# Optimization experiments

Measured on AMD Instinct MI355X. Metric: run time of the kernel, lower is better.

## Reference

```python
import jax, jax.numpy as jnp
import numpy as np

H = 2048            # hidden_size
HK, HV = 16, 32     # num_k_heads, num_v_heads
DK, DV = 128, 128   # head dims
KEY_DIM = HK * DK   # 2048
VAL_DIM = HV * DV   # 4096
CONV_DIM = 2 * KEY_DIM + VAL_DIM  # 8192
KW = 4              # conv kernel width
CS = 64             # chunk size
B, S = 2, 4096
EPS = 1e-6


def setup_inputs() -> dict:
    key = jax.random.key(0)
    ks = jax.random.split(key, 8)
    sc = lambda n: 1.0 / np.sqrt(n)
    return {
        "hidden_states": jax.random.normal(ks[0], (B, S, H), jnp.float32),
        "W_qkvz": jax.random.normal(ks[1], (H, 2 * KEY_DIM + 2 * VAL_DIM), jnp.float32) * sc(H),
        "W_ba": jax.random.normal(ks[2], (H, 2 * HV), jnp.float32) * sc(H),
        "conv_w": jax.random.normal(ks[3], (CONV_DIM, KW), jnp.float32) * sc(KW),
        "A_log": jnp.log(jax.random.uniform(ks[4], (HV,), jnp.float32, 1.0, 16.0)),
        "dt_bias": jax.random.normal(ks[5], (HV,), jnp.float32) * 0.1,
        "norm_weight": jnp.ones((DV,), jnp.float32),
        "W_out": jax.random.normal(ks[6], (VAL_DIM, H), jnp.float32) * sc(VAL_DIM),
    }


def l2norm(x, eps=1e-6):
    return x * jax.lax.rsqrt(jnp.sum(x * x, -1, keepdims=True) + eps)


def chunk_gated_delta_rule(q, k, v, g, beta):
    # q,k: (B,S,HV,DK); v: (B,S,HV,DV); g,beta: (B,S,HV). S divisible by CS.
    q = l2norm(q)
    k = l2norm(k)
    tr = lambda x: jnp.swapaxes(x, 1, 2).astype(jnp.float32)  # -> (B,H,S,...)
    q, k, v = tr(q), tr(k), tr(v)
    g = jnp.swapaxes(g, 1, 2).astype(jnp.float32)
    beta = jnp.swapaxes(beta, 1, 2).astype(jnp.float32)
    q = q * (1.0 / np.sqrt(DK))
    nc = S // CS
    rs = lambda x: x.reshape(B, HV, nc, CS, x.shape[-1])
    v_beta = v * beta[..., None]
    k_beta = k * beta[..., None]
    q, k, v, k_beta, v_beta = map(rs, (q, k, v, k_beta, v_beta))
    g = jnp.cumsum(g.reshape(B, HV, nc, CS), -1)
    tril = jnp.tril(jnp.ones((CS, CS), bool))
    diff = g[..., :, None] - g[..., None, :]
    decay = jnp.exp(jnp.where(tril, diff, 0.0)) * tril  # (B,H,nc,CS,CS)
    # strictly-lower A; the original sequential loop computes T = (I - A)^{-1}
    A = -jnp.tril(jnp.einsum('bhcid,bhcjd->bhcij', k_beta, k) * decay, -1)
    eye = jnp.eye(CS, dtype=jnp.float32)
    T = jax.scipy.linalg.solve_triangular(
        eye - A, jnp.broadcast_to(eye, A.shape), lower=True, unit_diagonal=True)
    v_t = jnp.einsum('bhcij,bhcjd->bhcid', T, v_beta)
    k_cumdecay = jnp.einsum('bhcij,bhcjd->bhcid', T, k_beta * jnp.exp(g)[..., None])
    strict_low = jnp.tril(jnp.ones((CS, CS), jnp.float32), -1)

    def step(state, xs):
        q_i, k_i, v_i, kc_i, g_i, dm_i = xs  # (B,H,CS,*)
        attn = jnp.einsum('bhid,bhjd->bhij', q_i, k_i) * dm_i * strict_low
        v_new = v_i - kc_i @ state
        out = (q_i * jnp.exp(g_i)[..., None]) @ state + attn @ v_new
        g_last = g_i[..., -1]
        state = state * jnp.exp(g_last)[..., None, None] + jnp.einsum(
            'bhcd,bhcv->bhdv', k_i * jnp.exp(g_last[..., None] - g_i)[..., None], v_new)
        return state, out

    S0 = jnp.zeros((B, HV, DK, DV), jnp.float32)
    mv = lambda x: jnp.moveaxis(x, 2, 0)  # chunk axis first for scan
    _, outs = jax.lax.scan(step, S0, (mv(q), mv(k), mv(v_t), mv(k_cumdecay), mv(g), mv(decay)))
    out = jnp.moveaxis(outs, 0, 2).reshape(B, HV, S, DV)
    return jnp.swapaxes(out, 1, 2)  # (B,S,HV,DV)


def reference(hidden_states, W_qkvz, W_ba, conv_w, A_log, dt_bias, norm_weight, W_out):
    r = HV // HK
    qkvz = hidden_states @ W_qkvz                     # (B,S,2*KEY+2*VAL)
    ba = hidden_states @ W_ba                         # (B,S,2*HV)
    qkvz = qkvz.reshape(B, S, HK, 2 * DK + 2 * r * DV)
    q, k, v, z = jnp.split(qkvz, [DK, 2 * DK, 2 * DK + r * DV], axis=-1)
    v = v.reshape(B, S, HV, DV)
    z = z.reshape(B, S, HV, DV)
    ba = ba.reshape(B, S, HK, 2 * r)
    b, a = jnp.split(ba, [r], axis=-1)
    b = b.reshape(B, S, HV)
    a = a.reshape(B, S, HV)
    # fused causal depthwise conv + silu over [q|k|v]
    mixed = jnp.concatenate([q.reshape(B, S, -1), k.reshape(B, S, -1), v.reshape(B, S, -1)], -1)
    x = jnp.swapaxes(mixed, 1, 2)                     # (B, CONV_DIM, S)
    xp = jnp.pad(x, ((0, 0), (0, 0), (KW - 1, 0)))
    conv = sum(conv_w[:, j][None, :, None] * xp[:, :, j:j + S] for j in range(KW))
    conv = jax.nn.silu(conv)
    qkv = jnp.swapaxes(conv, 1, 2)
    q, k, v = jnp.split(qkv, [KEY_DIM, 2 * KEY_DIM], axis=-1)
    q = q.reshape(B, S, HK, DK)
    k = k.reshape(B, S, HK, DK)
    v = v.reshape(B, S, HV, DV)
    beta = jax.nn.sigmoid(b)
    g = -jnp.exp(A_log) * jax.nn.softplus(a + dt_bias)
    q = jnp.repeat(q, r, axis=2)
    k = jnp.repeat(k, r, axis=2)
    core = chunk_gated_delta_rule(q, k, v, g, beta)   # (B,S,HV,DV)
    # gated RMSNorm over head_v_dim
    cf = core.astype(jnp.float32)
    var = jnp.mean(cf * cf, -1, keepdims=True)
    core = cf * jax.lax.rsqrt(var + EPS) * norm_weight
    core = core * jax.nn.silu(z.astype(jnp.float32))
    return core.reshape(B, S, VAL_DIM) @ W_out        # (B,S,H)
```

## Files before the change

### kernel.cpp

```cpp
#include <hip/hip_runtime.h>
#include <cstdint>
#include <cstddef>


typedef _Float16 half_t;
typedef _Float16 half2_t __attribute__((ext_vector_type(2)));
typedef _Float16 half4_t __attribute__((ext_vector_type(4)));
typedef _Float16 half8   __attribute__((ext_vector_type(8)));
typedef float    f32x4   __attribute__((ext_vector_type(4)));

#define MFMA16(a, b, c) __builtin_amdgcn_mfma_f32_16x16x32_f16((a), (b), (c), 0, 0, 0)

#define AS1 __attribute__((address_space(1)))
#define AS3 __attribute__((address_space(3)))

__device__ __forceinline__ void gload16(void* lds, const void* g) {
    __builtin_amdgcn_global_load_lds((AS1 void*)(g), (AS3 void*)(lds), 16, 0, 0);
}

__device__ __forceinline__ void at_wr(float* AT, int i, int j, float v) {
    *(float*)((char*)AT + i * 256 + ((j * 4) ^ ((i & 7) << 4))) = v;
}
__device__ __forceinline__ half8 frag64(const half_t* base, int row, int koff) {
    return *(const half8*)((const char*)base + row * 128 + ((koff * 2) ^ ((row & 7) << 4)));
}
__device__ __forceinline__ void w64(half_t* base, int row, int col, float v) {
    *(half_t*)((char*)base + row * 128 + ((col * 2) ^ ((row & 7) << 4))) = (half_t)v;
}
__device__ __forceinline__ half8 frag128(const half_t* base, int row, int koff) {
    return *(const half8*)((const char*)base + row * 256 + ((koff * 2) ^ ((row & 7) << 4)));
}

__global__ __launch_bounds__(256) void cast_h_k(const float* __restrict__ src,
                                                half_t* __restrict__ dst) {
    long i = (long)blockIdx.x * 256 + threadIdx.x;
    f32x4 v = *(const f32x4*)(src + i * 4);
    half4_t h;
    h[0] = (half_t)v[0]; h[1] = (half_t)v[1]; h[2] = (half_t)v[2]; h[3] = (half_t)v[3];
    *(half4_t*)(dst + i * 4) = h;
}

__global__ __launch_bounds__(256) void build_w1t_k(const float* __restrict__ Wq,
                                                   const float* __restrict__ Wba,
                                                   half_t* __restrict__ W1T) {
    __shared__ half_t tile[32][33];
    int n0 = blockIdx.x * 32, k0 = blockIdx.y * 32;
    int tx = threadIdx.x & 31, ty = threadIdx.x >> 5;
#pragma unroll
    for (int t = 0; t < 4; ++t) {
        int k = k0 + ty + t * 8, n = n0 + tx;
        float v = 0.f;
        if (n < 2048) {
            int kh = n >> 7, d = n & 127;
            v = Wq[(long)k * 12288 + kh * 768 + d];
        } else if (n < 4096) {
            int n2 = n - 2048; int kh = n2 >> 7, d = n2 & 127;
            v = Wq[(long)k * 12288 + kh * 768 + 128 + d];
        } else if (n < 8192) {
            int n3 = n - 4096; int vh = n3 >> 7, d = n3 & 127;
            int kh = vh >> 1, jj = vh & 1;
            v = Wq[(long)k * 12288 + kh * 768 + 256 + jj * 128 + d];
        } else if (n < 8256) {
            v = Wba[(long)k * 64 + (n - 8192)];
        } else if (n >= 8448) {
            int n4 = n - 8448; int vh = n4 >> 7, d = n4 & 127;
            int kh = vh >> 1, jj = vh & 1;
            v = Wq[(long)k * 12288 + kh * 768 + 512 + jj * 128 + d];
        }
        tile[ty + t * 8][tx] = (half_t)v;
    }
    __syncthreads();
#pragma unroll
    for (int t = 0; t < 4; ++t) {
        int n = n0 + ty + t * 8, k = k0 + tx;
        W1T[(long)n * 2048 + k] = tile[tx][ty + t * 8];
    }
}

__global__ __launch_bounds__(256) void build_wot_k(const float* __restrict__ Wo,
                                                   half_t* __restrict__ WoT) {
    __shared__ half_t tile[32][33];
    int n0 = blockIdx.x * 32, k0 = blockIdx.y * 32;
    int tx = threadIdx.x & 31, ty = threadIdx.x >> 5;
#pragma unroll
    for (int t = 0; t < 4; ++t) {
        int k = k0 + ty + t * 8, n = n0 + tx;
        tile[ty + t * 8][tx] = (half_t)Wo[(long)k * 2048 + n];
    }
    __syncthreads();
#pragma unroll
    for (int t = 0; t < 4; ++t) {
        int n = n0 + ty + t * 8, k = k0 + tx;
        WoT[(long)n * 4096 + k] = tile[tx][ty + t * 8];
    }
}

template <int OUT_F16>
__global__ __launch_bounds__(512, 2) void gemm256_k(const half_t* __restrict__ A,
                                                    const half_t* __restrict__ Bt,
                                                    void* __restrict__ C,
                                                    int K, int ldc,
                                                    int nwgM, int nwgN) {
    __shared__ half_t LA[2][2][8192];
    __shared__ half_t LB[2][2][8192];
    const int tid = threadIdx.x, lane = tid & 63, w = tid >> 6;
    const int lo = lane & 15, hi = lane >> 4;
    const int wm = w >> 2, wn = w & 3;
    const int nwg = gridDim.x, q = nwg >> 3, bid = blockIdx.x;
    const int swz = (bid & 7) * q + (bid >> 3);
    const int grp = 8 * nwgN;
    const int gid = swz / grp;
    const int rem = swz - gid * grp;
    const int fm = gid * 8;
    const int gsz = min(nwgM - fm, 8);
    const long tm = fm + rem % gsz;
    const long tn = rem / gsz;
    const long Kb = (long)K * 2;
    const char* Ab = (const char*)A + tm * 256 * Kb;
    const char* Bb = (const char*)Bt + tn * 256 * Kb;
    const int scol = ((lane & 7) << 4) ^ ((lane >> 3) << 4);
    const int srow = lane >> 3;
    const int s0 = w * 2, s1 = w * 2 + 1;

    auto stA = [&](int kt, int h) {
        char* hb = (char*)&LA[kt & 1][h][0];
        const char* gb = Ab + (long)(h * 128) * Kb + (long)kt * 128;
        gload16(hb + s0 * 1024, gb + (long)(s0 * 8 + srow) * Kb + scol);
        gload16(hb + s1 * 1024, gb + (long)(s1 * 8 + srow) * Kb + scol);
    };
    auto stB = [&](int kt, int h) {
        char* hb = (char*)&LB[kt & 1][h][0];
        const char* gb = Bb + (long)(h * 128) * Kb + (long)kt * 128;
        gload16(hb + s0 * 1024, gb + (long)(s0 * 8 + srow) * Kb + scol);
        gload16(hb + s1 * 1024, gb + (long)(s1 * 8 + srow) * Kb + scol);
    };
    auto rdA = [&](int p, int mt, int ks) -> half8 {
        int r = mt * 16 + lo;
        return *(const half8*)((const char*)&LA[p][wm][0] + r * 128 +
                               ((ks * 64 + hi * 16) ^ ((r & 7) << 4)));
    };
    auto rdB = [&](int p, int nt, int ks) -> half8 {
        int r = (wn & 1) * 64 + nt * 16 + lo;
        return *(const half8*)((const char*)&LB[p][wn >> 1][0] + r * 128 +
                               ((ks * 64 + hi * 16) ^ ((r & 7) << 4)));
    };

    f32x4 acc[8][4] = {};
    half8 af[4][2], bfa[2][2], bfb[2][2];

    auto ldsA4 = [&](int p, int mbase) {
#pragma unroll
        for (int mt = 0; mt < 4; ++mt) {
            af[mt][0] = rdA(p, mbase + mt, 0);
            af[mt][1] = rdA(p, mbase + mt, 1);
        }
    };
    auto ldsB2 = [&](int p, int nbase, half8 (&dst)[2][2]) {
#pragma unroll
        for (int nt = 0; nt < 2; ++nt) {
            dst[nt][0] = rdB(p, nbase + nt, 0);
            dst[nt][1] = rdB(p, nbase + nt, 1);
        }
    };
    auto quad = [&](const half8 (&bq)[2][2], int mo, int no) {
        __builtin_amdgcn_s_setprio(1);
#pragma unroll
        for (int mt = 0; mt < 4; ++mt)
#pragma unroll
            for (int nt = 0; nt < 2; ++nt) {
                acc[mo + mt][no + nt] = MFMA16(af[mt][0], bq[nt][0], acc[mo + mt][no + nt]);
                acc[mo + mt][no + nt] = MFMA16(af[mt][1], bq[nt][1], acc[mo + mt][no + nt]);
            }
        __builtin_amdgcn_s_setprio(0);
        __builtin_amdgcn_s_barrier();
    };

    const int nkt = K >> 6, niter = nkt >> 1;
    stA(0, 0); stA(0, 1); stB(0, 0); stB(0, 1);
    stA(1, 0); stB(1, 0); stB(1, 1);
    asm volatile("s_waitcnt vmcnt(6)" ::: "memory");
    __builtin_amdgcn_s_barrier();

    for (int i = 0; i < niter; ++i) {
        const int k0 = 2 * i, k1 = 2 * i + 1;
        const bool sa = (k0 + 2 < nkt), sb = (k1 + 2 < nkt);
        ldsA4(0, 0); ldsB2(0, 0, bfa);
        stA(k1, 1);
        __builtin_amdgcn_s_barrier();
        quad(bfa, 0, 0);
        ldsB2(0, 2, bfb);
        __builtin_amdgcn_s_barrier();
        quad(bfb, 0, 2);
        ldsA4(0, 4);
        if (sa) stB(k0 + 2, 0);
        __builtin_amdgcn_s_barrier();
        quad(bfa, 4, 0);
        if (sa) {
            stA(k0 + 2, 0); stB(k0 + 2, 1);
            asm volatile("s_waitcnt vmcnt(6)" ::: "memory");
        } else {
            asm volatile("s_waitcnt vmcnt(0)" ::: "memory");
        }
        __builtin_amdgcn_s_barrier();
        quad(bfb, 4, 2);
        ldsA4(1, 0); ldsB2(1, 0, bfa);
        if (sa) stA(k0 + 2, 1);
        __builtin_amdgcn_s_barrier();
        quad(bfa, 0, 0);
        ldsB2(1, 2, bfb);
        __builtin_amdgcn_s_barrier();
        quad(bfb, 0, 2);
        ldsA4(1, 4);
        if (sb) stB(k1 + 2, 0);
        __builtin_amdgcn_s_barrier();
        quad(bfa, 4, 0);
        if (sb) {
            stA(k1 + 2, 0); stB(k1 + 2, 1);
            asm volatile("s_waitcnt vmcnt(6)" ::: "memory");
        }
        __builtin_amdgcn_s_barrier();
        quad(bfb, 4, 2);
    }

    const long crow0 = tm * 256 + wm * 128 + hi * 4;
    const long ccol0 = tn * 256 + wn * 64 + lo;
#pragma unroll
    for (int mt = 0; mt < 8; ++mt)
#pragma unroll
        for (int nt = 0; nt < 4; ++nt)
#pragma unroll
            for (int e = 0; e < 4; ++e) {
                long row = crow0 + mt * 16 + e;
                long col = ccol0 + nt * 16;
                if (OUT_F16)
                    ((half_t*)C)[row * (long)ldc + col] = (half_t)acc[mt][nt][e];
                else
                    ((float*)C)[row * (long)ldc + col] = acc[mt][nt][e];
            }
}

__global__ __launch_bounds__(256) void conv_silu_k(const half_t* __restrict__ mixedH,
                                                   const float* __restrict__ conv_w,
                                                   half_t* __restrict__ qb,
                                                   half_t* __restrict__ kb,
                                                   half_t* __restrict__ vb) {
    int ch = blockIdx.x * 256 + threadIdx.x;
    int b = blockIdx.y >> 5, sc = blockIdx.y & 31;
    int s0 = sc * 128;
    half_t* dptr;
    long dstr;
    if (ch < 2048)      { dptr = qb + ch;          dstr = 2048; }
    else if (ch < 4096) { dptr = kb + (ch - 2048); dstr = 2048; }
    else                { dptr = vb + (ch - 4096); dstr = 4096; }
    float w0 = conv_w[ch * 4 + 0], w1 = conv_w[ch * 4 + 1];
    float w2 = conv_w[ch * 4 + 2], w3 = conv_w[ch * 4 + 3];
    const half_t* src = mixedH + (long)b * 4096 * 8448 + ch;
    float x0 = (s0 >= 3) ? (float)src[(long)(s0 - 3) * 8448] : 0.f;
    float x1 = (s0 >= 2) ? (float)src[(long)(s0 - 2) * 8448] : 0.f;
    float x2 = (s0 >= 1) ? (float)src[(long)(s0 - 1) * 8448] : 0.f;
    for (int s = s0; s < s0 + 128; ++s) {
        float x3 = (float)src[(long)s * 8448];
        float y = w0 * x0 + w1 * x1 + w2 * x2 + w3 * x3;
        y = y / (1.f + expf(-y));
        dptr[((long)b * 4096 + s) * dstr] = (half_t)y;
        x0 = x1; x1 = x2; x2 = x3;
    }
}

__global__ __launch_bounds__(256) void gate_beta_k(const half_t* __restrict__ mixedH,
                                                   const float* __restrict__ A_log,
                                                   const float* __restrict__ dt_bias,
                                                   float* __restrict__ beta,
                                                   float* __restrict__ gcum) {
    __shared__ float gs[32][64];
    int b = blockIdx.x >> 6, c = blockIdx.x & 63;
    for (int idx = threadIdx.x; idx < 2048; idx += 256) {
        int vh = idx & 31, i = idx >> 5;
        int kh = vh >> 1, j = vh & 1;
        long row = ((long)b * 4096 + c * 64 + i) * 8448 + 8192 + kh * 4;
        float bb = (float)mixedH[row + j];
        float aa = (float)mixedH[row + 2 + j];
        beta[((long)b * 4096 + c * 64 + i) * 32 + vh] = 1.f / (1.f + expf(-bb));
        float x = aa + dt_bias[vh];
        float sp = (x > 15.f) ? x : log1pf(expf(x));
        gs[vh][i] = -expf(A_log[vh]) * sp;
    }
    __syncthreads();
    if (threadIdx.x < 32) {
        int vh = threadIdx.x;
        float cum = 0.f;
        float* gout = gcum + ((long)(b * 32 + vh)) * 4096 + c * 64;
        for (int i = 0; i < 64; ++i) { cum += gs[vh][i]; gout[i] = cum; }
    }
}

__global__ __launch_bounds__(256) void l2norm_k(half_t* __restrict__ qb,
                                                half_t* __restrict__ kb) {
    int w = threadIdx.x >> 6, lane = threadIdx.x & 63;
    long rid = (long)blockIdx.x * 4 + w;
    half_t* base;
    float sc;
    if (rid < 131072) { base = qb + rid * 128; sc = 0.08838834764831845f; }
    else              { base = kb + (rid - 131072) * 128; sc = 1.f; }
    half2_t hv = *(half2_t*)(base + lane * 2);
    float f0 = (float)hv[0], f1 = (float)hv[1];
    float ss = f0 * f0 + f1 * f1;
#pragma unroll
    for (int off = 32; off; off >>= 1) ss += __shfl_xor(ss, off);
    float r = rsqrtf(ss + 1e-6f) * sc;
    half2_t o; o[0] = (half_t)(f0 * r); o[1] = (half_t)(f1 * r);
    *(half2_t*)(base + lane * 2) = o;
}

__global__ __launch_bounds__(256) void phase1_k(const half_t* __restrict__ qb,
                                                const half_t* __restrict__ kb,
                                                const half_t* __restrict__ vb,
                                                const float* __restrict__ beta,
                                                const float* __restrict__ gcum,
                                                half_t* __restrict__ attnW,
                                                half_t* __restrict__ vtW,
                                                half_t* __restrict__ kcW) {
    __shared__ float AT[64 * 64];
    __shared__ half_t XT[256 * 64];
    __shared__ float gcS[64], betaS[64], egS[64];
    int blk = blockIdx.x;
    int c = blk & 63, vh = (blk >> 6) & 31, b = blk >> 11;
    int kh = vh >> 1;
    int tid = threadIdx.x, lane = tid & 63, w = tid >> 6, lo = lane & 15, hi = lane >> 4;
    long rowbase = (long)b * 4096 + c * 64;
    if (tid < 64) {
        float g = gcum[((long)(b * 32 + vh)) * 4096 + c * 64 + tid];
        gcS[tid] = g; egS[tid] = expf(g);
        betaS[tid] = beta[(rowbase + tid) * 32 + vh];
    }
    const half_t* kR = kb + rowbase * 2048 + kh * 128;
    const half_t* qR = qb + rowbase * 2048 + kh * 128;
    f32x4 accG[4] = {}, accA[4] = {};
#pragma unroll
    for (int kt = 0; kt < 4; ++kt) {
        half8 ak = *(const half8*)(kR + (long)(w * 16 + lo) * 2048 + kt * 32 + hi * 8);
        half8 aq = *(const half8*)(qR + (long)(w * 16 + lo) * 2048 + kt * 32 + hi * 8);
#pragma unroll
        for (int n = 0; n < 4; ++n) {
            half8 bk = *(const half8*)(kR + (long)(n * 16 + lo) * 2048 + kt * 32 + hi * 8);
            accG[n] = MFMA16(ak, bk, accG[n]);
            accA[n] = MFMA16(aq, bk, accA[n]);
        }
    }
    __syncthreads();
    half_t* attnB = attnW + (long)blk * 4096;
#pragma unroll
    for (int n = 0; n < 4; ++n)
#pragma unroll
        for (int e = 0; e < 4; ++e) {
            int i = w * 16 + hi * 4 + e;
            int j = n * 16 + lo;
            float dec = (j < i) ? expf(gcS[i] - gcS[j]) : 0.f;
            float av = (j < i) ? (-betaS[i] * accG[n][e] * dec) : (j == i ? 1.f : 0.f);
            at_wr(AT, i, j, av);
            attnB[(long)i * 64 + j] = (half_t)((j < i) ? accA[n][e] * dec : 0.f);
        }
    __syncthreads();
    if (w == 0) {
        float t[64];
#pragma unroll
        for (int i = 0; i < 64; ++i) t[i] = (lane == i) ? 1.f : 0.f;
#pragma unroll
        for (int i = 1; i < 64; ++i) {
            float a0 = 0.f, a1 = 0.f, a2 = 0.f, a3 = 0.f;
#pragma unroll
            for (int p0 = 0; p0 < i; p0 += 4) {
                f32x4 a4 = *(const f32x4*)((const char*)AT + i * 256 +
                                           ((p0 * 4) ^ ((i & 7) << 4)));
                if (p0 + 0 < i) a0 += a4[0] * t[p0 + 0];
                if (p0 + 1 < i) a1 += a4[1] * t[p0 + 1];
                if (p0 + 2 < i) a2 += a4[2] * t[p0 + 2];
                if (p0 + 3 < i) a3 += a4[3] * t[p0 + 3];
            }
            t[i] += (a0 + a1) + (a2 + a3);
        }
        half_t* TS = (half_t*)AT;
#pragma unroll
        for (int i = 0; i < 64; ++i)
            *(half_t*)((char*)TS + i * 128 + ((lane * 2) ^ ((i & 7) << 4))) = (half_t)t[i];
    } else {
        for (int idx = tid - 64; idx < 4096; idx += 192) {
            int p = idx >> 6, dp = idx & 63;
            float bb = betaS[p], be = betaS[p] * egS[p];
            half2_t vv = *(const half2_t*)(vb + (rowbase + p) * 4096 + vh * 128 + dp * 2);
            half2_t kk = *(const half2_t*)(kb + (rowbase + p) * 2048 + kh * 128 + dp * 2);
            w64(XT, dp * 2,       p, (float)vv[0] * bb);
            w64(XT, dp * 2 + 1,   p, (float)vv[1] * bb);
            w64(XT, 128 + dp * 2,     p, (float)kk[0] * be);
            w64(XT, 128 + dp * 2 + 1, p, (float)kk[1] * be);
        }
    }
    __syncthreads();
    const half_t* TS = (const half_t*)AT;
    f32x4 accO[4][4] = {};
#pragma unroll
    for (int kt = 0; kt < 2; ++kt) {
        half8 tf[4];
#pragma unroll
        for (int m = 0; m < 4; ++m) tf[m] = frag64(TS, m * 16 + lo, kt * 32 + hi * 8);
#pragma unroll
        for (int n = 0; n < 4; ++n) {
            half8 bx = frag64(XT, w * 64 + n * 16 + lo, kt * 32 + hi * 8);
#pragma unroll
            for (int m = 0; m < 4; ++m) accO[m][n] = MFMA16(tf[m], bx, accO[m][n]);
        }
    }
    long ob = (long)blk * 8192;
#pragma unroll
    for (int m = 0; m < 4; ++m)
#pragma unroll
        for (int n = 0; n < 4; ++n)
#pragma unroll
            for (int e = 0; e < 4; ++e) {
                int i = m * 16 + hi * 4 + e;
                int dc = w * 64 + n * 16 + lo;
                float v = accO[m][n][e];
                if (dc < 128) vtW[ob + (long)i * 128 + dc] = (half_t)v;
                else          kcW[ob + (long)i * 128 + dc - 128] = (half_t)(-v);
            }
}

struct P2Ops {
    half8 kcf[4], qf[4], k8[4];
    half8 atf[2];
    half_t vtv[8];
    float gm, gi, g63;
};

__global__ __launch_bounds__(256, 1) void phase2_k(const half_t* __restrict__ qb,
                                                   const half_t* __restrict__ kb,
                                                   const float* __restrict__ gcum,
                                                   const half_t* __restrict__ attnW,
                                                   const half_t* __restrict__ vtW,
                                                   const half_t* __restrict__ kcW,
                                                   half_t* __restrict__ coreH) {
    __shared__ half_t SHs[32 * 128];
    __shared__ half_t vnT[32 * 64];
    __shared__ half_t kdT[128 * 64];
    int blk = blockIdx.x;
    int bvh = blk & 63, js = blk >> 6;
    int vh = bvh & 31, b = bvh >> 5, kh = vh >> 1;
    int j0 = js * 32;
    int tid = threadIdx.x, lane = tid & 63, w = tid >> 6, lo = lane & 15, hi = lane >> 4;
    int ii = tid >> 2, dseg = tid & 3;
    int jm = w >> 1, dql = (w & 1) * 4;
    for (int idx = tid; idx < 32 * 128; idx += 256) SHs[idx] = (half_t)0.f;
    __syncthreads();
    const float* gbase = gcum + (long)bvh * 4096;

    auto loadops = [&](int c, P2Ops& o) {
        long pb = (long)bvh * 64 + c;
        const half_t* kcG = kcW + pb * 8192;
        const half_t* vtG = vtW + pb * 8192;
        const half_t* atG = attnW + pb * 4096;
        long rowbase = (long)b * 4096 + c * 64;
        const float* gp = gbase + c * 64;
#pragma unroll
        for (int kt = 0; kt < 4; ++kt) {
            o.kcf[kt] = *(const half8*)(kcG + (long)(w * 16 + lo) * 128 + kt * 32 + hi * 8);
            o.qf[kt] = *(const half8*)(qb + (rowbase + w * 16 + lo) * 2048 + kh * 128 +
                                       kt * 32 + hi * 8);
        }
#pragma unroll
        for (int kt2 = 0; kt2 < 2; ++kt2)
            o.atf[kt2] = *(const half8*)(atG + (long)(w * 16 + lo) * 64 + kt2 * 32 + hi * 8);
#pragma unroll
        for (int s = 0; s < 4; ++s)
            o.k8[s] = *(const half8*)(kb + (rowbase + ii) * 2048 + kh * 128 + dseg * 32 + s * 8);
#pragma unroll
        for (int n = 0; n < 2; ++n)
#pragma unroll
            for (int e = 0; e < 4; ++e)
                o.vtv[n * 4 + e] = vtG[(long)(w * 16 + hi * 4 + e) * 128 + j0 + n * 16 + lo];
        o.gm = gp[w * 16 + lo];
        o.gi = gp[ii];
        o.g63 = gp[63];
    };

    auto step = [&](int c, P2Ops& o, P2Ops& nx) {
        long rowbase = (long)b * 4096 + c * 64;
        loadops(c + 1 < 64 ? c + 1 : 63, nx);
        half8 bS[4][2];
#pragma unroll
        for (int kt = 0; kt < 4; ++kt) {
            bS[kt][0] = frag128(SHs, lo, kt * 32 + hi * 8);
            bS[kt][1] = frag128(SHs, 16 + lo, kt * 32 + hi * 8);
        }
        f32x4 accV[2];
#pragma unroll
        for (int n = 0; n < 2; ++n)
#pragma unroll
            for (int e = 0; e < 4; ++e) accV[n][e] = (float)o.vtv[n * 4 + e];
#pragma unroll
        for (int kt = 0; kt < 4; ++kt) {
            accV[0] = MFMA16(o.kcf[kt], bS[kt][0], accV[0]);
            accV[1] = MFMA16(o.kcf[kt], bS[kt][1], accV[1]);
        }
#pragma unroll
        for (int n = 0; n < 2; ++n) {
            int j = n * 16 + lo, i0 = w * 16 + hi * 4;
            half4_t h4;
            h4[0] = (half_t)accV[n][0]; h4[1] = (half_t)accV[n][1];
            h4[2] = (half_t)accV[n][2]; h4[3] = (half_t)accV[n][3];
            *(half4_t*)((char*)vnT + j * 128 + ((i0 * 2) ^ ((j & 7) << 4))) = h4;
        }
        {
            float ek = expf(o.g63 - o.gi);
#pragma unroll
            for (int s = 0; s < 4; ++s)
#pragma unroll
                for (int e2 = 0; e2 < 8; ++e2)
                    w64(kdT, dseg * 32 + s * 8 + e2, ii, (float)o.k8[s][e2] * ek);
        }
        __syncthreads();
        float egm = expf(o.gm);
        f32x4 accO[2] = {};
#pragma unroll
        for (int kt = 0; kt < 4; ++kt) {
            half8 aq;
#pragma unroll
            for (int e2 = 0; e2 < 8; ++e2) aq[e2] = (half_t)((float)o.qf[kt][e2] * egm);
            accO[0] = MFMA16(aq, bS[kt][0], accO[0]);
            accO[1] = MFMA16(aq, bS[kt][1], accO[1]);
        }
#pragma unroll
        for (int kt2 = 0; kt2 < 2; ++kt2) {
            half8 bV0 = frag64(vnT, lo, kt2 * 32 + hi * 8);
            half8 bV1 = frag64(vnT, 16 + lo, kt2 * 32 + hi * 8);
            accO[0] = MFMA16(o.atf[kt2], bV0, accO[0]);
            accO[1] = MFMA16(o.atf[kt2], bV1, accO[1]);
        }
        f32x4 accU[4] = {};
#pragma unroll
        for (int kt2 = 0; kt2 < 2; ++kt2) {
            half8 avn = frag64(vnT, jm * 16 + lo, kt2 * 32 + hi * 8);
#pragma unroll
            for (int dnn = 0; dnn < 4; ++dnn) {
                half8 bkd = frag64(kdT, (dql + dnn) * 16 + lo, kt2 * 32 + hi * 8);
                accU[dnn] = MFMA16(avn, bkd, accU[dnn]);
            }
        }
#pragma unroll
        for (int n = 0; n < 2; ++n)
#pragma unroll
            for (int e = 0; e < 4; ++e)
                coreH[(rowbase + w * 16 + hi * 4 + e) * 4096 + vh * 128 + j0 + n * 16 + lo] =
                    (half_t)accO[n][e];
        __syncthreads();
        float egl = expf(o.g63);
#pragma unroll
        for (int dnn = 0; dnn < 4; ++dnn)
#pragma unroll
            for (int e = 0; e < 4; ++e) {
                int j = jm * 16 + hi * 4 + e;
                int d = (dql + dnn) * 16 + lo;
                char* p = (char*)SHs + j * 256 + ((d * 2) ^ ((j & 7) << 4));
                float old = (float)*(half_t*)p;
                *(half_t*)p = (half_t)(old * egl + accU[dnn][e]);
            }
        __syncthreads();
    };

    P2Ops opsA, opsB;
    loadops(0, opsA);
    for (int c = 0; c < 64; c += 2) {
        step(c, opsA, opsB);
        step(c + 1, opsB, opsA);
    }
}

__global__ __launch_bounds__(256) void normgate_k(half_t* __restrict__ coreH,
                                                  const half_t* __restrict__ zH,
                                                  const float* __restrict__ norm_w) {
    int w = threadIdx.x >> 6, lane = threadIdx.x & 63;
    long rid = (long)blockIdx.x * 4 + w;
    long bs = rid >> 5;
    int vh = rid & 31;
    half_t* cr = coreH + bs * 4096 + vh * 128;
    half2_t cv = *(half2_t*)(cr + lane * 2);
    float f0 = (float)cv[0], f1 = (float)cv[1];
    float ss = f0 * f0 + f1 * f1;
#pragma unroll
    for (int off = 32; off; off >>= 1) ss += __shfl_xor(ss, off);
    float rs = rsqrtf(ss * (1.f / 128.f) + 1e-6f);
    half2_t zz = *(const half2_t*)(zH + bs * 4096 + vh * 128 + lane * 2);
    float z0 = (float)zz[0], z1 = (float)zz[1];
    float s0 = z0 / (1.f + expf(-z0)), s1 = z1 / (1.f + expf(-z1));
    float w0 = norm_w[lane * 2], w1 = norm_w[lane * 2 + 1];
    half2_t o;
    o[0] = (half_t)(f0 * rs * w0 * s0);
    o[1] = (half_t)(f1 * rs * w1 * s1);
    *(half2_t*)(cr + lane * 2) = o;
}

extern "C" void kernel_launch(void* const* d_in, const int* in_sizes, int n_in,
                              void* d_out, int out_size, void* d_ws, size_t ws_size,
                              hipStream_t stream) {
    const float* hidden  = (const float*)d_in[0];
    const float* W_qkvz  = (const float*)d_in[1];
    const float* W_ba    = (const float*)d_in[2];
    const float* conv_w  = (const float*)d_in[3];
    const float* A_log   = (const float*)d_in[4];
    const float* dt_bias = (const float*)d_in[5];
    const float* norm_w  = (const float*)d_in[6];
    const float* W_out   = (const float*)d_in[7];
    float* out = (float*)d_out;

    char* ws = (char*)d_ws;
    const size_t MB = 1ull << 20;
    half_t* qb      = (half_t*)(ws + 0);
    half_t* kb      = (half_t*)(ws + 32 * MB);
    half_t* vb      = (half_t*)(ws + 64 * MB);
    float*  betaB   = (float*) (ws + 128 * MB);
    float*  gcum    = (float*) (ws + 129 * MB);
    half_t* WoT     = (half_t*)(ws + 130 * MB);
    half_t* zH      = (half_t*)(ws + 146 * MB);
    half_t* mixedH  = (half_t*)(ws + 210 * MB);
    half_t* attnW   = (half_t*)(ws + 210 * MB);
    half_t* vtW     = (half_t*)(ws + 242 * MB);
    half_t* kcW     = (half_t*)(ws + 306 * MB);
    half_t* hiddenH = (half_t*)(ws + 0);
    half_t* W1T     = (half_t*)(ws + 32 * MB);
    half_t* coreH   = (half_t*)(ws + 64 * MB);
    (void)ws_size; (void)in_sizes; (void)n_in; (void)out_size;

    cast_h_k<<<16384, 256, 0, stream>>>(hidden, hiddenH);
    build_w1t_k<<<dim3(392, 64), 256, 0, stream>>>(W_qkvz, W_ba, W1T);
    build_wot_k<<<dim3(64, 128), 256, 0, stream>>>(W_out, WoT);
    gemm256_k<1><<<32 * 33, 512, 0, stream>>>(hiddenH, W1T, mixedH, 2048, 8448, 32, 33);
    gemm256_k<1><<<32 * 16, 512, 0, stream>>>(hiddenH, W1T + (size_t)8448 * 2048, zH,
                                              2048, 4096, 32, 16);
    conv_silu_k<<<dim3(32, 64), 256, 0, stream>>>(mixedH, conv_w, qb, kb, vb);
    gate_beta_k<<<128, 256, 0, stream>>>(mixedH, A_log, dt_bias, betaB, gcum);
    l2norm_k<<<65536, 256, 0, stream>>>(qb, kb);
    phase1_k<<<4096, 256, 0, stream>>>(qb, kb, vb, betaB, gcum, attnW, vtW, kcW);
    phase2_k<<<256, 256, 0, stream>>>(qb, kb, gcum, attnW, vtW, kcW, coreH);
    normgate_k<<<65536, 256, 0, stream>>>(coreH, zH, norm_w);
    gemm256_k<0><<<32 * 8, 512, 0, stream>>>(coreH, WoT, out, 4096, 2048, 32, 8);
}
```

Baseline: 1.207 ms.

## Split ba projection into small GEMM, prefetch B fragments, use fast exp

The 64 b/a columns move out of the padded 8448-wide main projection GEMM into a dedicated small MFMA kernel. This removes the 33rd tile column, which was mostly padding, and makes the mixed buffer 8192 wide. The GEMM main loop now issues the first B-fragment LDS read of each half-iteration earlier, before the preceding barrier, to overlap LDS latency with MFMA work. All expf calls become __expf, trading a little accuracy for cheaper transcendentals.

```diff
diff --git a/kernel.cpp b/kernel.cpp
--- a/kernel.cpp
+++ b/kernel.cpp
@@ -60,12 +60,12 @@
             int n3 = n - 4096; int vh = n3 >> 7, d = n3 & 127;
             int kh = vh >> 1, jj = vh & 1;
             v = Wq[(long)k * 12288 + kh * 768 + 256 + jj * 128 + d];
-        } else if (n < 8256) {
-            v = Wba[(long)k * 64 + (n - 8192)];
-        } else if (n >= 8448) {
-            int n4 = n - 8448; int vh = n4 >> 7, d = n4 & 127;
+        } else if (n < 12288) {
+            int n4 = n - 8192; int vh = n4 >> 7, d = n4 & 127;
             int kh = vh >> 1, jj = vh & 1;
             v = Wq[(long)k * 12288 + kh * 768 + 512 + jj * 128 + d];
+        } else if (n < 12352) {
+            v = Wba[(long)k * 64 + (n - 12288)];
         }
         tile[ty + t * 8][tx] = (half_t)v;
     }
@@ -180,11 +180,12 @@
     stA(1, 0); stB(1, 0); stB(1, 1);
     asm volatile("s_waitcnt vmcnt(6)" ::: "memory");
     __builtin_amdgcn_s_barrier();
+    ldsB2(0, 0, bfa);
 
     for (int i = 0; i < niter; ++i) {
         const int k0 = 2 * i, k1 = 2 * i + 1;
         const bool sa = (k0 + 2 < nkt), sb = (k1 + 2 < nkt);
-        ldsA4(0, 0); ldsB2(0, 0, bfa);
+        ldsA4(0, 0);
         stA(k1, 1);
         __builtin_amdgcn_s_barrier();
         quad(bfa, 0, 0);
@@ -201,9 +202,10 @@
         } else {
             asm volatile("s_waitcnt vmcnt(0)" ::: "memory");
         }
+        ldsB2(1, 0, bfa);
         __builtin_amdgcn_s_barrier();
         quad(bfb, 4, 2);
-        ldsA4(1, 0); ldsB2(1, 0, bfa);
+        ldsA4(1, 0);
         if (sa) stA(k0 + 2, 1);
         __builtin_amdgcn_s_barrier();
         quad(bfa, 0, 0);
@@ -218,6 +220,7 @@
             stA(k1 + 2, 0); stB(k1 + 2, 1);
             asm volatile("s_waitcnt vmcnt(6)" ::: "memory");
         }
+        if (i + 1 < niter) ldsB2(0, 0, bfa);
         __builtin_amdgcn_s_barrier();
         quad(bfb, 4, 2);
     }
@@ -237,6 +240,31 @@
                 else
                     ((float*)C)[row * (long)ldc + col] = acc[mt][nt][e];
             }
+}
+
+__global__ __launch_bounds__(256) void ba_gemm_k(const half_t* __restrict__ A,
+                                                 const half_t* __restrict__ Bt,
+                                                 half_t* __restrict__ baH) {
+    int tid = threadIdx.x, lane = tid & 63, w = tid >> 6;
+    int lo = lane & 15, hi = lane >> 4;
+    int mt = w >> 1, np = w & 1;
+    long rb = (long)blockIdx.x * 32;
+    f32x4 acc[2] = {};
+    for (int kk = 0; kk < 64; ++kk) {
+        half8 a = *(const half8*)(A + (rb + mt * 16 + lo) * 2048 + kk * 32 + hi * 8);
+#pragma unroll
+        for (int j = 0; j < 2; ++j) {
+            half8 b = *(const half8*)(Bt + (long)(np * 32 + j * 16 + lo) * 2048 +
+                                      kk * 32 + hi * 8);
+            acc[j] = MFMA16(a, b, acc[j]);
+        }
+    }
+#pragma unroll
+    for (int j = 0; j < 2; ++j)
+#pragma unroll
+        for (int e = 0; e < 4; ++e)
+            baH[(rb + mt * 16 + hi * 4 + e) * 64 + np * 32 + j * 16 + lo] =
+                (half_t)acc[j][e];
 }
 
 __global__ __launch_bounds__(256) void conv_silu_k(const half_t* __restrict__ mixedH,
@@ -254,20 +282,20 @@
     else                { dptr = vb + (ch - 4096); dstr = 4096; }
     float w0 = conv_w[ch * 4 + 0], w1 = conv_w[ch * 4 + 1];
     float w2 = conv_w[ch * 4 + 2], w3 = conv_w[ch * 4 + 3];
-    const half_t* src = mixedH + (long)b * 4096 * 8448 + ch;
-    float x0 = (s0 >= 3) ? (float)src[(long)(s0 - 3) * 8448] : 0.f;
-    float x1 = (s0 >= 2) ? (float)src[(long)(s0 - 2) * 8448] : 0.f;
-    float x2 = (s0 >= 1) ? (float)src[(long)(s0 - 1) * 8448] : 0.f;
+    const half_t* src = mixedH + (long)b * 4096 * 8192 + ch;
+    float x0 = (s0 >= 3) ? (float)src[(long)(s0 - 3) * 8192] : 0.f;
+    float x1 = (s0 >= 2) ? (float)src[(long)(s0 - 2) * 8192] : 0.f;
+    float x2 = (s0 >= 1) ? (float)src[(long)(s0 - 1) * 8192] : 0.f;
     for (int s = s0; s < s0 + 128; ++s) {
-        float x3 = (float)src[(long)s * 8448];
+        float x3 = (float)src[(long)s * 8192];
         float y = w0 * x0 + w1 * x1 + w2 * x2 + w3 * x3;
-        y = y / (1.f + expf(-y));
+        y = y / (1.f + __expf(-y));
         dptr[((long)b * 4096 + s) * dstr] = (half_t)y;
         x0 = x1; x1 = x2; x2 = x3;
     }
 }
 
-__global__ __launch_bounds__(256) void gate_beta_k(const half_t* __restrict__ mixedH,
+__global__ __launch_bounds__(256) void gate_beta_k(const half_t* __restrict__ baH,
                                                    const float* __restrict__ A_log,
                                                    const float* __restrict__ dt_bias,
                                                    float* __restrict__ beta,
@@ -277,13 +305,13 @@
     for (int idx = threadIdx.x; idx < 2048; idx += 256) {
         int vh = idx & 31, i = idx >> 5;
         int kh = vh >> 1, j = vh & 1;
-        long row = ((long)b * 4096 + c * 64 + i) * 8448 + 8192 + kh * 4;
-        float bb = (float)mixedH[row + j];
-        float aa = (float)mixedH[row + 2 + j];
-        beta[((long)b * 4096 + c * 64 + i) * 32 + vh] = 1.f / (1.f + expf(-bb));
+        long row = ((long)b * 4096 + c * 64 + i) * 64 + kh * 4;
+        float bb = (float)baH[row + j];
+        float aa = (float)baH[row + 2 + j];
+        beta[((long)b * 4096 + c * 64 + i) * 32 + vh] = 1.f / (1.f + __expf(-bb));
         float x = aa + dt_bias[vh];
-        float sp = (x > 15.f) ? x : log1pf(expf(x));
-        gs[vh][i] = -expf(A_log[vh]) * sp;
+        float sp = (x > 15.f) ? x : log1pf(__expf(x));
+        gs[vh][i] = -__expf(A_log[vh]) * sp;
     }
     __syncthreads();
     if (threadIdx.x < 32) {
@@ -330,7 +358,7 @@
     long rowbase = (long)b * 4096 + c * 64;
     if (tid < 64) {
         float g = gcum[((long)(b * 32 + vh)) * 4096 + c * 64 + tid];
-        gcS[tid] = g; egS[tid] = expf(g);
+        gcS[tid] = g; egS[tid] = __expf(g);
         betaS[tid] = beta[(rowbase + tid) * 32 + vh];
     }
     const half_t* kR = kb + rowbase * 2048 + kh * 128;
@@ -355,7 +383,7 @@
         for (int e = 0; e < 4; ++e) {
             int i = w * 16 + hi * 4 + e;
             int j = n * 16 + lo;
-            float dec = (j < i) ? expf(gcS[i] - gcS[j]) : 0.f;
+            float dec = (j < i) ? __expf(gcS[i] - gcS[j]) : 0.f;
             float av = (j < i) ? (-betaS[i] * accG[n][e] * dec) : (j == i ? 1.f : 0.f);
             at_wr(AT, i, j, av);
             attnB[(long)i * 64 + j] = (half_t)((j < i) ? accA[n][e] * dec : 0.f);
@@ -510,7 +538,7 @@
             *(half4_t*)((char*)vnT + j * 128 + ((i0 * 2) ^ ((j & 7) << 4))) = h4;
         }
         {
-            float ek = expf(o.g63 - o.gi);
+            float ek = __expf(o.g63 - o.gi);
 #pragma unroll
             for (int s = 0; s < 4; ++s)
 #pragma unroll
@@ -518,7 +546,7 @@
                     w64(kdT, dseg * 32 + s * 8 + e2, ii, (float)o.k8[s][e2] * ek);
         }
         __syncthreads();
-        float egm = expf(o.gm);
+        float egm = __expf(o.gm);
         f32x4 accO[2] = {};
 #pragma unroll
         for (int kt = 0; kt < 4; ++kt) {
@@ -552,7 +580,7 @@
                 coreH[(rowbase + w * 16 + hi * 4 + e) * 4096 + vh * 128 + j0 + n * 16 + lo] =
                     (half_t)accO[n][e];
         __syncthreads();
-        float egl = expf(o.g63);
+        float egl = __expf(o.g63);
 #pragma unroll
         for (int dnn = 0; dnn < 4; ++dnn)
 #pragma unroll
@@ -590,7 +618,7 @@
     float rs = rsqrtf(ss * (1.f / 128.f) + 1e-6f);
     half2_t zz = *(const half2_t*)(zH + bs * 4096 + vh * 128 + lane * 2);
     float z0 = (float)zz[0], z1 = (float)zz[1];
-    float s0 = z0 / (1.f + expf(-z0)), s1 = z1 / (1.f + expf(-z1));
+    float s0 = z0 / (1.f + __expf(-z0)), s1 = z1 / (1.f + __expf(-z1));
     float w0 = norm_w[lane * 2], w1 = norm_w[lane * 2 + 1];
     half2_t o;
     o[0] = (half_t)(f0 * rs * w0 * s0);
@@ -624,6 +652,7 @@
     half_t* attnW   = (half_t*)(ws + 210 * MB);
     half_t* vtW     = (half_t*)(ws + 242 * MB);
     half_t* kcW     = (half_t*)(ws + 306 * MB);
+    half_t* baH     = (half_t*)(ws + 338 * MB);
     half_t* hiddenH = (half_t*)(ws + 0);
     half_t* W1T     = (half_t*)(ws + 32 * MB);
     half_t* coreH   = (half_t*)(ws + 64 * MB);
@@ -632,14 +661,15 @@
     cast_h_k<<<16384, 256, 0, stream>>>(hidden, hiddenH);
     build_w1t_k<<<dim3(392, 64), 256, 0, stream>>>(W_qkvz, W_ba, W1T);
     build_wot_k<<<dim3(64, 128), 256, 0, stream>>>(W_out, WoT);
-    gemm256_k<1><<<32 * 33, 512, 0, stream>>>(hiddenH, W1T, mixedH, 2048, 8448, 32, 33);
-    gemm256_k<1><<<32 * 16, 512, 0, stream>>>(hiddenH, W1T + (size_t)8448 * 2048, zH,
-                                              2048, 4096, 32, 16);
+    gemm256_k<1><<<1024, 512, 0, stream>>>(hiddenH, W1T, mixedH, 2048, 8192, 32, 32);
+    gemm256_k<1><<<512, 512, 0, stream>>>(hiddenH, W1T + (size_t)8192 * 2048, zH,
+                                          2048, 4096, 32, 16);
+    ba_gemm_k<<<256, 256, 0, stream>>>(hiddenH, W1T + (size_t)12288 * 2048, baH);
     conv_silu_k<<<dim3(32, 64), 256, 0, stream>>>(mixedH, conv_w, qb, kb, vb);
-    gate_beta_k<<<128, 256, 0, stream>>>(mixedH, A_log, dt_bias, betaB, gcum);
+    gate_beta_k<<<128, 256, 0, stream>>>(baH, A_log, dt_bias, betaB, gcum);
     l2norm_k<<<65536, 256, 0, stream>>>(qb, kb);
     phase1_k<<<4096, 256, 0, stream>>>(qb, kb, vb, betaB, gcum, attnW, vtW, kcW);
     phase2_k<<<256, 256, 0, stream>>>(qb, kb, gcum, attnW, vtW, kcW, coreH);
     normgate_k<<<65536, 256, 0, stream>>>(coreH, zH, norm_w);
-    gemm256_k<0><<<32 * 8, 512, 0, stream>>>(coreH, WoT, out, 4096, 2048, 32, 8);
-}
+    gemm256_k<0><<<256, 512, 0, stream>>>(coreH, WoT, out, 4096, 2048, 32, 8);
+}
```

After: 1.285 ms. +6.4%, slower.
